# Kernel optimization log

Hardware: AMD Instinct MI355X
Metric: run time of the kernel (lower is better)

Reference implementation:

```python
import jax, jax.numpy as jnp
import numpy as np

N = 100000      # nodes
E = 1600000     # directed edges (avg degree 16)
IN, HID, OUT = 128, 128, 64


def setup_inputs() -> dict:
    key = jax.random.key(0)
    ks = jax.random.split(key, 6)
    x = jax.random.normal(ks[0], (N, IN), dtype=jnp.float32)
    edge_index = jax.random.randint(ks[1], (2, E), 0, N, dtype=jnp.int32)
    W1 = jax.random.normal(ks[2], (IN, HID), dtype=jnp.float32) * (1.0 / np.sqrt(IN))
    b1 = jax.random.normal(ks[3], (HID,), dtype=jnp.float32) * 0.01
    W2 = jax.random.normal(ks[4], (HID, OUT), dtype=jnp.float32) * (1.0 / np.sqrt(HID))
    b2 = jax.random.normal(ks[5], (OUT,), dtype=jnp.float32) * 0.01
    return {"x": x, "edge_index": edge_index, "W1": W1, "b1": b1, "W2": W2, "b2": b2}


def _gcn_norm(edge_index):
    # add self-loops, compute symmetric normalization deg^-1/2 A_hat deg^-1/2
    loop = jnp.arange(N, dtype=edge_index.dtype)
    row = jnp.concatenate([edge_index[0], loop])  # source
    col = jnp.concatenate([edge_index[1], loop])  # target
    deg = jax.ops.segment_sum(jnp.ones(row.shape[0], jnp.float32), col, num_segments=N)
    dinv = jnp.where(deg > 0, jax.lax.rsqrt(deg), 0.0)
    norm = dinv[row] * dinv[col]  # [E+N]
    return row, col, norm


def _gcn_conv(x, row, col, norm, W, b):
    h = x @ W                              # [N, out] dense transform first (fewer features moved)
    msg = h[row] * norm[:, None]           # gather over edges
    agg = jax.ops.segment_sum(msg, col, num_segments=N)  # scatter-add to targets
    return agg + b


def reference(x, edge_index, W1, b1, W2, b2):
    row, col, norm = _gcn_norm(edge_index)
    h = jax.nn.relu(_gcn_conv(x, row, col, norm, W1, b1))
    return _gcn_conv(h, row, col, norm, W2, b2)
```

## Files before the change

kernel.cpp:

```cpp
#include <hip/hip_runtime.h>

#define NN 100000
#define NE 1600000
#define SCAN_B 1024

#define BSH 9
#define BSZ 512
#define NBUK 196
#define CAP 12288
#define CHUNK 4096

typedef _Float16 hs8 __attribute__((ext_vector_type(8)));
typedef float f32x4 __attribute__((ext_vector_type(4)));
typedef float f32x2 __attribute__((ext_vector_type(2)));
#define MFMA16H(a, b, c) __builtin_amdgcn_mfma_f32_16x16x32_f16(a, b, c, 0, 0, 0)

static inline size_t alignup(size_t x) { return (x + 255) & ~(size_t)255; }

union h8u { uint4 q; _Float16 h[8]; };


__global__ __launch_bounds__(256) void k_prep0(int* __restrict__ gcur,
                                               const float* __restrict__ W1, _Float16* __restrict__ WT1,
                                               const float* __restrict__ W2, _Float16* __restrict__ WT2) {
  int b = blockIdx.x, t = threadIdx.x;
  if (b < 64) {
    int i = b * 256 + t;
    int k = i >> 7, c = i & 127;
    WT1[c * 128 + k] = (_Float16)W1[i];
  } else if (b < 96) {
    int i = (b - 64) * 256 + t;
    int k = i >> 6, c = i & 63;
    WT2[c * 128 + k] = (_Float16)W2[i];
  } else {
    if (t < NBUK) gcur[t] = t * CAP;
  }
}

__global__ __launch_bounds__(256) void k_bucket(const int* __restrict__ row, const int* __restrict__ col,
                                                int* __restrict__ gcur, uint* __restrict__ pr_pack) {
  __shared__ int cnt[NBUK];
  int t = threadIdx.x;
  for (int i = t; i < NBUK; i += 256) cnt[i] = 0;
  __syncthreads();
  int e0 = blockIdx.x * CHUNK;
  int e1 = min(e0 + CHUNK, NE);
  for (int e = e0 + t; e < e1; e += 256) atomicAdd(&cnt[col[e] >> BSH], 1);
  __syncthreads();
  for (int i = t; i < NBUK; i += 256) {
    int c = cnt[i];
    cnt[i] = c ? atomicAdd(&gcur[i], c) : 0;
  }
  __syncthreads();
  for (int e = e0 + t; e < e1; e += 256) {
    int c = col[e];
    int p = atomicAdd(&cnt[c >> BSH], 1);
    pr_pack[p] = ((uint)row[e] << BSH) | (uint)(c & (BSZ - 1));
  }
}

__global__ __launch_bounds__(256) void k_bdeg(const uint* __restrict__ pr_pack, const int* __restrict__ gcur,
                                              int* __restrict__ deg, float* __restrict__ dinv) {
  __shared__ int dc[BSZ];
  int t = threadIdx.x, b = blockIdx.x;
  for (int i = t; i < BSZ; i += 256) dc[i] = 0;
  __syncthreads();
  int s = b * CAP;
  int n = min(gcur[b] - s, CAP);
  for (int i = t; i < n; i += 256) atomicAdd(&dc[pr_pack[s + i] & (BSZ - 1)], 1);
  __syncthreads();
  int nb0 = b << BSH;
  for (int i = t; i < BSZ; i += 256) {
    int node = nb0 + i;
    if (node < NN) {
      int d = dc[i] + 1;
      deg[node] = d;
      dinv[node] = rsqrtf((float)d);
    }
  }
}

__global__ __launch_bounds__(SCAN_B) void k_scan1(const int* __restrict__ deg, int* __restrict__ offs,
                                                  int* __restrict__ bsums) {
  __shared__ int sm[SCAN_B];
  int i = blockIdx.x * SCAN_B + threadIdx.x;
  int v = (i < NN) ? deg[i] : 0;
  sm[threadIdx.x] = v;
  __syncthreads();
  for (int d = 1; d < SCAN_B; d <<= 1) {
    int t = (threadIdx.x >= d) ? sm[threadIdx.x - d] : 0;
    __syncthreads();
    sm[threadIdx.x] += t;
    __syncthreads();
  }
  if (i < NN) offs[i] = sm[threadIdx.x] - v;
  if (threadIdx.x == SCAN_B - 1) bsums[blockIdx.x] = sm[threadIdx.x];
}

__global__ __launch_bounds__(128) void k_scan2(int* __restrict__ bsums, int nb) {
  __shared__ int sm[128];
  int v = (threadIdx.x < nb) ? bsums[threadIdx.x] : 0;
  sm[threadIdx.x] = v;
  __syncthreads();
  for (int d = 1; d < 128; d <<= 1) {
    int t = (threadIdx.x >= d) ? sm[threadIdx.x - d] : 0;
    __syncthreads();
    sm[threadIdx.x] += t;
    __syncthreads();
  }
  if (threadIdx.x < nb) bsums[threadIdx.x] = sm[threadIdx.x] - v;
}

__global__ __launch_bounds__(SCAN_B) void k_scan3(int* __restrict__ offs, const int* __restrict__ bsums) {
  int i = blockIdx.x * SCAN_B + threadIdx.x;
  if (i < NN) offs[i] += bsums[blockIdx.x];
}

__global__ __launch_bounds__(256) void k_bfill(const uint* __restrict__ pr_pack, const int* __restrict__ gcur,
                                               const int* __restrict__ offs, const float* __restrict__ dinv,
                                               uint2* __restrict__ wcsr) {
  __shared__ int loff[BSZ];
  __shared__ int cur[BSZ];
  __shared__ float dl[BSZ];
  int t = threadIdx.x, b = blockIdx.x;
  int nb0 = b << BSH;
  for (int i = t; i < BSZ; i += 256) {
    int node = nb0 + i;
    if (node < NN) {
      int o = offs[node];
      float d = dinv[node];
      loff[i] = o;
      dl[i] = d;
      cur[i] = 1;
      wcsr[o] = make_uint2((uint)node, __float_as_uint(d * d));
    } else {
      loff[i] = 0; dl[i] = 0.f; cur[i] = 1;
    }
  }
  __syncthreads();
  int s = b * CAP;
  int n = min(gcur[b] - s, CAP);
  for (int i = t; i < n; i += 256) {
    uint prk = pr_pack[s + i];
    int li = (int)(prk & (BSZ - 1));
    uint r = prk >> BSH;
    int p = atomicAdd(&cur[li], 1);
    wcsr[loff[li] + p] = make_uint2(r, __float_as_uint(dinv[r] * dl[li]));
  }
}


__global__ __launch_bounds__(256) void k_gemm128(const float* __restrict__ x, const _Float16* __restrict__ WT,
                                                 unsigned char* __restrict__ t8) {
  int wave = threadIdx.x >> 6, lane = threadIdx.x & 63;
  int col0 = wave * 32;
  int lr = lane & 15;
  int lk = (lane >> 4) * 8;
  hs8 bfrag[2][4];
#pragma unroll
  for (int n = 0; n < 2; n++)
#pragma unroll
    for (int ks = 0; ks < 4; ks++)
      bfrag[n][ks] = *(const hs8*)&WT[(size_t)(col0 + n * 16 + lr) * 128 + ks * 32 + lk];
  int row0 = blockIdx.x * 64;
#pragma unroll 1
  for (int mt = 0; mt < 4; mt++) {
    int r0 = row0 + mt * 16;
    if (r0 >= NN) return;
    const float* xr = x + (size_t)(r0 + lr) * 128 + lk;
    f32x4 acc[2] = {{0.f, 0.f, 0.f, 0.f}, {0.f, 0.f, 0.f, 0.f}};
#pragma unroll
    for (int ks = 0; ks < 4; ks++) {
      float4 a0 = *(const float4*)&xr[ks * 32];
      float4 a1 = *(const float4*)&xr[ks * 32 + 4];
      hs8 af;
      af[0] = (_Float16)a0.x; af[1] = (_Float16)a0.y;
      af[2] = (_Float16)a0.z; af[3] = (_Float16)a0.w;
      af[4] = (_Float16)a1.x; af[5] = (_Float16)a1.y;
      af[6] = (_Float16)a1.z; af[7] = (_Float16)a1.w;
      acc[0] = MFMA16H(af, bfrag[0][ks], acc[0]);
      acc[1] = MFMA16H(af, bfrag[1][ks], acc[1]);
    }
    int rbase = r0 + (lane >> 4) * 4;
#pragma unroll
    for (int n = 0; n < 2; n++)
#pragma unroll
      for (int r = 0; r < 4; r++) {
        uint e = (uint)__builtin_amdgcn_cvt_pk_fp8_f32(acc[n][r], acc[n][r], 0, false);
        t8[(size_t)(rbase + r) * 128 + col0 + n * 16 + lr] = (unsigned char)(e & 0xffu);
      }
  }
}

__global__ __launch_bounds__(256) void k_gemm64(const _Float16* __restrict__ h, const _Float16* __restrict__ WT,
                                                _Float16* __restrict__ t2) {
  int wave = threadIdx.x >> 6, lane = threadIdx.x & 63;
  int col0 = wave * 16;
  int lr = lane & 15;
  int lk = (lane >> 4) * 8;
  hs8 bfrag[4];
#pragma unroll
  for (int ks = 0; ks < 4; ks++)
    bfrag[ks] = *(const hs8*)&WT[(size_t)(col0 + lr) * 128 + ks * 32 + lk];
  int row0 = blockIdx.x * 64;
#pragma unroll 1
  for (int mt = 0; mt < 4; mt++) {
    int r0 = row0 + mt * 16;
    if (r0 >= NN) return;
    const _Float16* hr = h + (size_t)(r0 + lr) * 128 + lk;
    f32x4 acc = {0.f, 0.f, 0.f, 0.f};
#pragma unroll
    for (int ks = 0; ks < 4; ks++) {
      hs8 af = *(const hs8*)&hr[ks * 32];
      acc = MFMA16H(af, bfrag[ks], acc);
    }
    int rbase = r0 + (lane >> 4) * 4;
#pragma unroll
    for (int r = 0; r < 4; r++)
      t2[(size_t)(rbase + r) * 64 + col0 + lr] = (_Float16)acc[r];
  }
}


__global__ __launch_bounds__(256) void k_agg128(const unsigned char* __restrict__ t8, const int* __restrict__ offs,
                                                const int* __restrict__ deg, const uint2* __restrict__ wcsr,
                                                const float* __restrict__ bias, _Float16* __restrict__ out) {
  int wave = threadIdx.x >> 6, lane = threadIdx.x & 63;
  int node = blockIdx.x * 4 + wave;
  if (node >= NN) return;
  int g = lane >> 4, f = lane & 15;
  float acc[8] = {};
  int beg = offs[node];
  int cnt = deg[node];
  const char* tb = (const char*)t8;
  for (int base = 0; base < cnt; base += 64) {
    int m = min(64, cnt - base);
    uint2 pr = (lane < m) ? wcsr[beg + base + lane] : make_uint2(0u, 0u);
    int ridx = (int)pr.x;
    float wv = __uint_as_float(pr.y);
    int mm = (m + 3) >> 2;
    for (int k = 0; k < mm; k++) {
      int src = k * 4 + g;
      int r = __shfl(ridx, src);
      float s = __shfl(wv, src);
      uint2 u = *(const uint2*)(tb + (((size_t)(uint)r) << 7) + (f << 3));
      f32x2 p0 = __builtin_amdgcn_cvt_pk_f32_fp8(u.x, false);
      f32x2 p1 = __builtin_amdgcn_cvt_pk_f32_fp8(u.x, true);
      f32x2 p2 = __builtin_amdgcn_cvt_pk_f32_fp8(u.y, false);
      f32x2 p3 = __builtin_amdgcn_cvt_pk_f32_fp8(u.y, true);
      acc[0] = fmaf(p0[0], s, acc[0]);
      acc[1] = fmaf(p0[1], s, acc[1]);
      acc[2] = fmaf(p1[0], s, acc[2]);
      acc[3] = fmaf(p1[1], s, acc[3]);
      acc[4] = fmaf(p2[0], s, acc[4]);
      acc[5] = fmaf(p2[1], s, acc[5]);
      acc[6] = fmaf(p3[0], s, acc[6]);
      acc[7] = fmaf(p3[1], s, acc[7]);
    }
  }
#pragma unroll
  for (int j = 0; j < 8; j++) {
    acc[j] += __shfl_xor(acc[j], 16);
    acc[j] += __shfl_xor(acc[j], 32);
  }
  if (g == 0) {
    float4 b0 = *(const float4*)&bias[f * 8];
    float4 b1 = *(const float4*)&bias[f * 8 + 4];
    h8u st;
    st.h[0] = (_Float16)fmaxf(acc[0] + b0.x, 0.f);
    st.h[1] = (_Float16)fmaxf(acc[1] + b0.y, 0.f);
    st.h[2] = (_Float16)fmaxf(acc[2] + b0.z, 0.f);
    st.h[3] = (_Float16)fmaxf(acc[3] + b0.w, 0.f);
    st.h[4] = (_Float16)fmaxf(acc[4] + b1.x, 0.f);
    st.h[5] = (_Float16)fmaxf(acc[5] + b1.y, 0.f);
    st.h[6] = (_Float16)fmaxf(acc[6] + b1.z, 0.f);
    st.h[7] = (_Float16)fmaxf(acc[7] + b1.w, 0.f);
    *(uint4*)&out[(size_t)node * 128 + f * 8] = st.q;
  }
}

__global__ __launch_bounds__(256) void k_agg64(const _Float16* __restrict__ t, const int* __restrict__ offs,
                                               const int* __restrict__ deg, const uint2* __restrict__ wcsr,
                                               const float* __restrict__ bias, float* __restrict__ out) {
  int wave = threadIdx.x >> 6, lane = threadIdx.x & 63;
  int node = blockIdx.x * 4 + wave;
  if (node >= NN) return;
  int g = lane >> 3, fl = lane & 7;
  float acc[8] = {};
  int beg = offs[node];
  int cnt = deg[node];
  const char* tb = (const char*)t;
  for (int base = 0; base < cnt; base += 64) {
    int m = min(64, cnt - base);
    uint2 pr = (lane < m) ? wcsr[beg + base + lane] : make_uint2(0u, 0u);
    int ridx = (int)pr.x;
    float wv = __uint_as_float(pr.y);
    int mm = (m + 7) >> 3;
    for (int k = 0; k < mm; k++) {
      int src = k * 8 + g;
      int r = __shfl(ridx, src);
      float s = __shfl(wv, src);
      h8u u;
      u.q = *(const uint4*)(tb + (((size_t)(uint)r) << 7) + (fl << 4));
      acc[0] = fmaf((float)u.h[0], s, acc[0]);
      acc[1] = fmaf((float)u.h[1], s, acc[1]);
      acc[2] = fmaf((float)u.h[2], s, acc[2]);
      acc[3] = fmaf((float)u.h[3], s, acc[3]);
      acc[4] = fmaf((float)u.h[4], s, acc[4]);
      acc[5] = fmaf((float)u.h[5], s, acc[5]);
      acc[6] = fmaf((float)u.h[6], s, acc[6]);
      acc[7] = fmaf((float)u.h[7], s, acc[7]);
    }
  }
#pragma unroll
  for (int j = 0; j < 8; j++) {
    acc[j] += __shfl_xor(acc[j], 8);
    acc[j] += __shfl_xor(acc[j], 16);
    acc[j] += __shfl_xor(acc[j], 32);
  }
  if (g == 0) {
    float4 b0 = *(const float4*)&bias[fl * 8];
    float4 b1 = *(const float4*)&bias[fl * 8 + 4];
    float4 o0 = make_float4(acc[0] + b0.x, acc[1] + b0.y, acc[2] + b0.z, acc[3] + b0.w);
    float4 o1 = make_float4(acc[4] + b1.x, acc[5] + b1.y, acc[6] + b1.z, acc[7] + b1.w);
    *(float4*)&out[(size_t)node * 64 + fl * 8] = o0;
    *(float4*)&out[(size_t)node * 64 + fl * 8 + 4] = o1;
  }
}


extern "C" void kernel_launch(void* const* d_in, const int* in_sizes, int n_in,
                              void* d_out, int out_size, void* d_ws, size_t ws_size,
                              hipStream_t stream) {
  const float* x  = (const float*)d_in[0];
  const int*   ei = (const int*)d_in[1];
  const float* W1 = (const float*)d_in[2];
  const float* b1 = (const float*)d_in[3];
  const float* W2 = (const float*)d_in[4];
  const float* b2 = (const float*)d_in[5];
  float* out = (float*)d_out;

  char* p = (char*)d_ws;
  int* deg       = (int*)p;      p += alignup((size_t)NN * 4);
  int* gcur      = (int*)p;      p += alignup((size_t)NBUK * 4);
  int* offs      = (int*)p;      p += alignup((size_t)NN * 4);
  int* bsums     = (int*)p;      p += alignup(128 * 4);
  float* dinv    = (float*)p;    p += alignup((size_t)NN * 4);
  uint2* wcsr    = (uint2*)p;    p += alignup((size_t)(NE + NN + 64) * 8);
  _Float16* WT1  = (_Float16*)p; p += alignup(128 * 128 * 2);
  _Float16* WT2  = (_Float16*)p; p += alignup(64 * 128 * 2);
  unsigned char* t8 = (unsigned char*)p; p += alignup((size_t)NN * 128);
  _Float16* t2   = (_Float16*)p; p += alignup((size_t)NN * 64 * 2);
  _Float16* h1   = (_Float16*)p; p += alignup((size_t)NN * 128 * 2);
  uint* pr_pack  = (uint*)t2;
  (void)ws_size; (void)in_sizes; (void)n_in; (void)out_size;

  const int* row = ei;
  const int* col = ei + NE;

  int nbScan = (NN + SCAN_B - 1) / SCAN_B;
  int nbB = (NE + CHUNK - 1) / CHUNK;

  k_prep0<<<97, 256, 0, stream>>>(gcur, W1, WT1, W2, WT2);
  k_bucket<<<nbB, 256, 0, stream>>>(row, col, gcur, pr_pack);
  k_bdeg<<<NBUK, 256, 0, stream>>>(pr_pack, gcur, deg, dinv);
  k_scan1<<<nbScan, SCAN_B, 0, stream>>>(deg, offs, bsums);
  k_scan2<<<1, 128, 0, stream>>>(bsums, nbScan);
  k_scan3<<<nbScan, SCAN_B, 0, stream>>>(offs, bsums);
  k_bfill<<<NBUK, 256, 0, stream>>>(pr_pack, gcur, offs, dinv, wcsr);

  int nbG = (NN + 63) / 64;
  k_gemm128<<<nbG, 256, 0, stream>>>(x, WT1, t8);
  k_agg128<<<NN / 4, 256, 0, stream>>>(t8, offs, deg, wcsr, b1, h1);
  k_gemm64<<<nbG, 256, 0, stream>>>(h1, WT2, t2);
  k_agg64<<<NN / 4, 256, 0, stream>>>(t2, offs, deg, wcsr, b2, out);
}
```

Baseline: 222.9 us.

## Fuse degree scan into bucket kernels and process two nodes per wave in aggregation

Replaces the three-kernel global prefix scan with per-bucket totals emitted by k_bdeg, a single 196-entry scan, and an in-block scan inside k_bfill that writes offs directly. This removes two launches and a pass over the node arrays. k_bucket now holds each thread's 16 edges in registers so row and col are read from global memory only once. Both aggregation kernels now assign half a wave per node and software-prefetch the next CSR entry instead of staging 64 edges and shuffling them, which raises node-level parallelism but puts fewer lanes on each high-degree node.

```diff
diff --git a/kernel.cpp b/kernel.cpp
--- a/kernel.cpp
+++ b/kernel.cpp
@@ -2,13 +2,13 @@
 
 #define NN 100000
 #define NE 1600000
-#define SCAN_B 1024
 
 #define BSH 9
 #define BSZ 512
 #define NBUK 196
 #define CAP 12288
 #define CHUNK 4096
+#define EPT 16
 
 typedef _Float16 hs8 __attribute__((ext_vector_type(8)));
 typedef float f32x4 __attribute__((ext_vector_type(4)));
@@ -44,23 +44,34 @@
   for (int i = t; i < NBUK; i += 256) cnt[i] = 0;
   __syncthreads();
   int e0 = blockIdx.x * CHUNK;
-  int e1 = min(e0 + CHUNK, NE);
-  for (int e = e0 + t; e < e1; e += 256) atomicAdd(&cnt[col[e] >> BSH], 1);
+  int rr[EPT], cc[EPT];
+#pragma unroll
+  for (int i = 0; i < EPT; i++) {
+    int e = e0 + t + i * 256;
+    bool ok = e < NE;
+    cc[i] = ok ? col[e] : -1;
+    rr[i] = ok ? row[e] : 0;
+  }
+#pragma unroll
+  for (int i = 0; i < EPT; i++)
+    if (cc[i] >= 0) atomicAdd(&cnt[cc[i] >> BSH], 1);
   __syncthreads();
   for (int i = t; i < NBUK; i += 256) {
     int c = cnt[i];
     cnt[i] = c ? atomicAdd(&gcur[i], c) : 0;
   }
   __syncthreads();
-  for (int e = e0 + t; e < e1; e += 256) {
-    int c = col[e];
-    int p = atomicAdd(&cnt[c >> BSH], 1);
-    pr_pack[p] = ((uint)row[e] << BSH) | (uint)(c & (BSZ - 1));
-  }
+#pragma unroll
+  for (int i = 0; i < EPT; i++)
+    if (cc[i] >= 0) {
+      int p = atomicAdd(&cnt[cc[i] >> BSH], 1);
+      pr_pack[p] = ((uint)rr[i] << BSH) | (uint)(cc[i] & (BSZ - 1));
+    }
 }
 
 __global__ __launch_bounds__(256) void k_bdeg(const uint* __restrict__ pr_pack, const int* __restrict__ gcur,
-                                              int* __restrict__ deg, float* __restrict__ dinv) {
+                                              int* __restrict__ deg, float* __restrict__ dinv,
+                                              int* __restrict__ bsums) {
   __shared__ int dc[BSZ];
   int t = threadIdx.x, b = blockIdx.x;
   for (int i = t; i < BSZ; i += 256) dc[i] = 0;
@@ -78,64 +89,63 @@
       dinv[node] = rsqrtf((float)d);
     }
   }
-}
-
-__global__ __launch_bounds__(SCAN_B) void k_scan1(const int* __restrict__ deg, int* __restrict__ offs,
-                                                  int* __restrict__ bsums) {
-  __shared__ int sm[SCAN_B];
-  int i = blockIdx.x * SCAN_B + threadIdx.x;
-  int v = (i < NN) ? deg[i] : 0;
-  sm[threadIdx.x] = v;
-  __syncthreads();
-  for (int d = 1; d < SCAN_B; d <<= 1) {
-    int t = (threadIdx.x >= d) ? sm[threadIdx.x - d] : 0;
+  if (t == 0) bsums[b] = n + min(BSZ, NN - nb0);
+}
+
+__global__ __launch_bounds__(256) void k_scanB(int* __restrict__ bsums) {
+  __shared__ int sm[256];
+  int t = threadIdx.x;
+  int v = (t < NBUK) ? bsums[t] : 0;
+  sm[t] = v;
+  __syncthreads();
+  for (int d = 1; d < 256; d <<= 1) {
+    int tmp = (t >= d) ? sm[t - d] : 0;
     __syncthreads();
-    sm[threadIdx.x] += t;
+    sm[t] += tmp;
     __syncthreads();
   }
-  if (i < NN) offs[i] = sm[threadIdx.x] - v;
-  if (threadIdx.x == SCAN_B - 1) bsums[blockIdx.x] = sm[threadIdx.x];
-}
-
-__global__ __launch_bounds__(128) void k_scan2(int* __restrict__ bsums, int nb) {
-  __shared__ int sm[128];
-  int v = (threadIdx.x < nb) ? bsums[threadIdx.x] : 0;
-  sm[threadIdx.x] = v;
-  __syncthreads();
-  for (int d = 1; d < 128; d <<= 1) {
-    int t = (threadIdx.x >= d) ? sm[threadIdx.x - d] : 0;
-    __syncthreads();
-    sm[threadIdx.x] += t;
-    __syncthreads();
-  }
-  if (threadIdx.x < nb) bsums[threadIdx.x] = sm[threadIdx.x] - v;
-}
-
-__global__ __launch_bounds__(SCAN_B) void k_scan3(int* __restrict__ offs, const int* __restrict__ bsums) {
-  int i = blockIdx.x * SCAN_B + threadIdx.x;
-  if (i < NN) offs[i] += bsums[blockIdx.x];
+  if (t < NBUK) bsums[t] = sm[t] - v;
 }
 
 __global__ __launch_bounds__(256) void k_bfill(const uint* __restrict__ pr_pack, const int* __restrict__ gcur,
-                                               const int* __restrict__ offs, const float* __restrict__ dinv,
+                                               const int* __restrict__ deg, const float* __restrict__ dinv,
+                                               const int* __restrict__ bsums, int* __restrict__ offs,
                                                uint2* __restrict__ wcsr) {
   __shared__ int loff[BSZ];
   __shared__ int cur[BSZ];
   __shared__ float dl[BSZ];
+  __shared__ int tsum[256];
   int t = threadIdx.x, b = blockIdx.x;
   int nb0 = b << BSH;
-  for (int i = t; i < BSZ; i += 256) {
-    int node = nb0 + i;
-    if (node < NN) {
-      int o = offs[node];
-      float d = dinv[node];
-      loff[i] = o;
-      dl[i] = d;
-      cur[i] = 1;
-      wcsr[o] = make_uint2((uint)node, __float_as_uint(d * d));
-    } else {
-      loff[i] = 0; dl[i] = 0.f; cur[i] = 1;
-    }
+  int i0 = 2 * t, i1 = i0 + 1;
+  int n0 = nb0 + i0, n1 = nb0 + i1;
+  int d0 = (n0 < NN) ? deg[n0] : 0;
+  int d1 = (n1 < NN) ? deg[n1] : 0;
+  int v = d0 + d1;
+  tsum[t] = v;
+  __syncthreads();
+  for (int d = 1; d < 256; d <<= 1) {
+    int tmp = (t >= d) ? tsum[t - d] : 0;
+    __syncthreads();
+    tsum[t] += tmp;
+    __syncthreads();
+  }
+  int base = bsums[b] + tsum[t] - v;
+  float dv0 = (n0 < NN) ? dinv[n0] : 0.f;
+  float dv1 = (n1 < NN) ? dinv[n1] : 0.f;
+  loff[i0] = base;
+  loff[i1] = base + d0;
+  dl[i0] = dv0;
+  dl[i1] = dv1;
+  cur[i0] = 1;
+  cur[i1] = 1;
+  if (n0 < NN) {
+    offs[n0] = base;
+    wcsr[base] = make_uint2((uint)n0, __float_as_uint(dv0 * dv0));
+  }
+  if (n1 < NN) {
+    offs[n1] = base + d0;
+    wcsr[base + d0] = make_uint2((uint)n1, __float_as_uint(dv1 * dv1));
   }
   __syncthreads();
   int s = b * CAP;
@@ -226,44 +236,39 @@
                                                 const int* __restrict__ deg, const uint2* __restrict__ wcsr,
                                                 const float* __restrict__ bias, _Float16* __restrict__ out) {
   int wave = threadIdx.x >> 6, lane = threadIdx.x & 63;
-  int node = blockIdx.x * 4 + wave;
-  if (node >= NN) return;
-  int g = lane >> 4, f = lane & 15;
+  int half = lane >> 5;
+  int sub = (lane >> 4) & 1;
+  int f = lane & 15;
+  int node = blockIdx.x * 8 + wave * 2 + half;
+  int beg = offs[node];
+  int d = deg[node];
+  const char* tb = (const char*)t8;
   float acc[8] = {};
-  int beg = offs[node];
-  int cnt = deg[node];
-  const char* tb = (const char*)t8;
-  for (int base = 0; base < cnt; base += 64) {
-    int m = min(64, cnt - base);
-    uint2 pr = (lane < m) ? wcsr[beg + base + lane] : make_uint2(0u, 0u);
-    int ridx = (int)pr.x;
-    float wv = __uint_as_float(pr.y);
-    int mm = (m + 3) >> 2;
-    for (int k = 0; k < mm; k++) {
-      int src = k * 4 + g;
-      int r = __shfl(ridx, src);
-      float s = __shfl(wv, src);
-      uint2 u = *(const uint2*)(tb + (((size_t)(uint)r) << 7) + (f << 3));
-      f32x2 p0 = __builtin_amdgcn_cvt_pk_f32_fp8(u.x, false);
-      f32x2 p1 = __builtin_amdgcn_cvt_pk_f32_fp8(u.x, true);
-      f32x2 p2 = __builtin_amdgcn_cvt_pk_f32_fp8(u.y, false);
-      f32x2 p3 = __builtin_amdgcn_cvt_pk_f32_fp8(u.y, true);
-      acc[0] = fmaf(p0[0], s, acc[0]);
-      acc[1] = fmaf(p0[1], s, acc[1]);
-      acc[2] = fmaf(p1[0], s, acc[2]);
-      acc[3] = fmaf(p1[1], s, acc[3]);
-      acc[4] = fmaf(p2[0], s, acc[4]);
-      acc[5] = fmaf(p2[1], s, acc[5]);
-      acc[6] = fmaf(p3[0], s, acc[6]);
-      acc[7] = fmaf(p3[1], s, acc[7]);
-    }
-  }
-#pragma unroll
-  for (int j = 0; j < 8; j++) {
-    acc[j] += __shfl_xor(acc[j], 16);
-    acc[j] += __shfl_xor(acc[j], 32);
-  }
-  if (g == 0) {
+  int trips = (d + 1) >> 1;
+  uint2 e = (sub < d) ? wcsr[beg + sub] : make_uint2(0u, 0u);
+#pragma unroll 1
+  for (int k = 0; k < trips; k++) {
+    int ns = (k + 1) * 2 + sub;
+    uint2 en = (ns < d) ? wcsr[beg + ns] : make_uint2(0u, 0u);
+    float s = __uint_as_float(e.y);
+    uint2 u = *(const uint2*)(tb + (((size_t)e.x) << 7) + (f << 3));
+    f32x2 p0 = __builtin_amdgcn_cvt_pk_f32_fp8(u.x, false);
+    f32x2 p1 = __builtin_amdgcn_cvt_pk_f32_fp8(u.x, true);
+    f32x2 p2 = __builtin_amdgcn_cvt_pk_f32_fp8(u.y, false);
+    f32x2 p3 = __builtin_amdgcn_cvt_pk_f32_fp8(u.y, true);
+    acc[0] = fmaf(p0[0], s, acc[0]);
+    acc[1] = fmaf(p0[1], s, acc[1]);
+    acc[2] = fmaf(p1[0], s, acc[2]);
+    acc[3] = fmaf(p1[1], s, acc[3]);
+    acc[4] = fmaf(p2[0], s, acc[4]);
+    acc[5] = fmaf(p2[1], s, acc[5]);
+    acc[6] = fmaf(p3[0], s, acc[6]);
+    acc[7] = fmaf(p3[1], s, acc[7]);
+    e = en;
+  }
+#pragma unroll
+  for (int j = 0; j < 8; j++) acc[j] += __shfl_xor(acc[j], 16);
+  if (sub == 0) {
     float4 b0 = *(const float4*)&bias[f * 8];
     float4 b1 = *(const float4*)&bias[f * 8 + 4];
     h8u st;
@@ -283,48 +288,45 @@
                                                const int* __restrict__ deg, const uint2* __restrict__ wcsr,
                                                const float* __restrict__ bias, float* __restrict__ out) {
   int wave = threadIdx.x >> 6, lane = threadIdx.x & 63;
-  int node = blockIdx.x * 4 + wave;
-  if (node >= NN) return;
-  int g = lane >> 3, fl = lane & 7;
+  int half = lane >> 5;
+  int sub = (lane >> 3) & 3;
+  int f8 = lane & 7;
+  int node = blockIdx.x * 8 + wave * 2 + half;
+  int beg = offs[node];
+  int d = deg[node];
+  const char* tb = (const char*)t;
   float acc[8] = {};
-  int beg = offs[node];
-  int cnt = deg[node];
-  const char* tb = (const char*)t;
-  for (int base = 0; base < cnt; base += 64) {
-    int m = min(64, cnt - base);
-    uint2 pr = (lane < m) ? wcsr[beg + base + lane] : make_uint2(0u, 0u);
-    int ridx = (int)pr.x;
-    float wv = __uint_as_float(pr.y);
-    int mm = (m + 7) >> 3;
-    for (int k = 0; k < mm; k++) {
-      int src = k * 8 + g;
-      int r = __shfl(ridx, src);
-      float s = __shfl(wv, src);
-      h8u u;
-      u.q = *(const uint4*)(tb + (((size_t)(uint)r) << 7) + (fl << 4));
-      acc[0] = fmaf((float)u.h[0], s, acc[0]);
-      acc[1] = fmaf((float)u.h[1], s, acc[1]);
-      acc[2] = fmaf((float)u.h[2], s, acc[2]);
-      acc[3] = fmaf((float)u.h[3], s, acc[3]);
-      acc[4] = fmaf((float)u.h[4], s, acc[4]);
-      acc[5] = fmaf((float)u.h[5], s, acc[5]);
-      acc[6] = fmaf((float)u.h[6], s, acc[6]);
-      acc[7] = fmaf((float)u.h[7], s, acc[7]);
-    }
+  int trips = (d + 3) >> 2;
+  uint2 e = (sub < d) ? wcsr[beg + sub] : make_uint2(0u, 0u);
+#pragma unroll 1
+  for (int k = 0; k < trips; k++) {
+    int ns = (k + 1) * 4 + sub;
+    uint2 en = (ns < d) ? wcsr[beg + ns] : make_uint2(0u, 0u);
+    float s = __uint_as_float(e.y);
+    h8u u;
+    u.q = *(const uint4*)(tb + (((size_t)e.x) << 7) + (f8 << 4));
+    acc[0] = fmaf((float)u.h[0], s, acc[0]);
+    acc[1] = fmaf((float)u.h[1], s, acc[1]);
+    acc[2] = fmaf((float)u.h[2], s, acc[2]);
+    acc[3] = fmaf((float)u.h[3], s, acc[3]);
+    acc[4] = fmaf((float)u.h[4], s, acc[4]);
+    acc[5] = fmaf((float)u.h[5], s, acc[5]);
+    acc[6] = fmaf((float)u.h[6], s, acc[6]);
+    acc[7] = fmaf((float)u.h[7], s, acc[7]);
+    e = en;
   }
 #pragma unroll
   for (int j = 0; j < 8; j++) {
     acc[j] += __shfl_xor(acc[j], 8);
     acc[j] += __shfl_xor(acc[j], 16);
-    acc[j] += __shfl_xor(acc[j], 32);
-  }
-  if (g == 0) {
-    float4 b0 = *(const float4*)&bias[fl * 8];
-    float4 b1 = *(const float4*)&bias[fl * 8 + 4];
+  }
+  if (sub == 0) {
+    float4 b0 = *(const float4*)&bias[f8 * 8];
+    float4 b1 = *(const float4*)&bias[f8 * 8 + 4];
     float4 o0 = make_float4(acc[0] + b0.x, acc[1] + b0.y, acc[2] + b0.z, acc[3] + b0.w);
     float4 o1 = make_float4(acc[4] + b1.x, acc[5] + b1.y, acc[6] + b1.z, acc[7] + b1.w);
-    *(float4*)&out[(size_t)node * 64 + fl * 8] = o0;
-    *(float4*)&out[(size_t)node * 64 + fl * 8 + 4] = o1;
+    *(float4*)&out[(size_t)node * 64 + f8 * 8] = o0;
+    *(float4*)&out[(size_t)node * 64 + f8 * 8 + 4] = o1;
   }
 }
 
@@ -344,7 +346,7 @@
   int* deg       = (int*)p;      p += alignup((size_t)NN * 4);
   int* gcur      = (int*)p;      p += alignup((size_t)NBUK * 4);
   int* offs      = (int*)p;      p += alignup((size_t)NN * 4);
-  int* bsums     = (int*)p;      p += alignup(128 * 4);
+  int* bsums     = (int*)p;      p += alignup(256 * 4);
   float* dinv    = (float*)p;    p += alignup((size_t)NN * 4);
   uint2* wcsr    = (uint2*)p;    p += alignup((size_t)(NE + NN + 64) * 8);
   _Float16* WT1  = (_Float16*)p; p += alignup(128 * 128 * 2);
@@ -358,20 +360,18 @@
   const int* row = ei;
   const int* col = ei + NE;
 
-  int nbScan = (NN + SCAN_B - 1) / SCAN_B;
   int nbB = (NE + CHUNK - 1) / CHUNK;
 
   k_prep0<<<97, 256, 0, stream>>>(gcur, W1, WT1, W2, WT2);
   k_bucket<<<nbB, 256, 0, stream>>>(row, col, gcur, pr_pack);
-  k_bdeg<<<NBUK, 256, 0, stream>>>(pr_pack, gcur, deg, dinv);
-  k_scan1<<<nbScan, SCAN_B, 0, stream>>>(deg, offs, bsums);
-  k_scan2<<<1, 128, 0, stream>>>(bsums, nbScan);
-  k_scan3<<<nbScan, SCAN_B, 0, stream>>>(offs, bsums);
-  k_bfill<<<NBUK, 256, 0, stream>>>(pr_pack, gcur, offs, dinv, wcsr);
+  k_bdeg<<<NBUK, 256, 0, stream>>>(pr_pack, gcur, deg, dinv, bsums);
+  k_scanB<<<1, 256, 0, stream>>>(bsums);
+  k_bfill<<<NBUK, 256, 0, stream>>>(pr_pack, gcur, deg, dinv, bsums, offs, wcsr);
 
   int nbG = (NN + 63) / 64;
+  int nbA = NN / 8;
   k_gemm128<<<nbG, 256, 0, stream>>>(x, WT1, t8);
-  k_agg128<<<NN / 4, 256, 0, stream>>>(t8, offs, deg, wcsr, b1, h1);
+  k_agg128<<<nbA, 256, 0, stream>>>(t8, offs, deg, wcsr, b1, h1);
   k_gemm64<<<nbG, 256, 0, stream>>>(h1, WT2, t2);
-  k_agg64<<<NN / 4, 256, 0, stream>>>(t2, offs, deg, wcsr, b2, out);
-}
+  k_agg64<<<nbA, 256, 0, stream>>>(t2, offs, deg, wcsr, b2, out);
+}
```

Result: faster. 195.5 us (-12.3%).
